# Kernel tuning notes

Measured on AMD Instinct MI355X. Metric: run time of the kernel, lower is better.

Reference implementation:

```python
import jax, jax.numpy as jnp
import numpy as np

LN_EPS = 1e-12


def setup_inputs() -> dict:
    key = jax.random.key(0)
    ks = jax.random.split(key, 6)
    B, S, H = 32, 512, 768
    P, K = 76, 64
    V, E = 50257, 768
    return {
        "sequence_data": jax.random.normal(ks[0], (B, S, H), dtype=jnp.float32),
        "masked_positions": jax.random.randint(ks[1], (B, P), 0, S, dtype=jnp.int64),
        "candidate_sets": jax.random.randint(ks[2], (B, P, K), 0, V, dtype=jnp.int64),
        "embedding_table": jax.random.normal(ks[3], (V, E), dtype=jnp.float32) * 0.02,
        "dense_w": jax.random.normal(ks[4], (H, E), dtype=jnp.float32) * (1.0 / np.sqrt(H)),
        "dense_b": jnp.zeros((E,), dtype=jnp.float32),
        "ln_gamma": jnp.ones((E,), dtype=jnp.float32),
        "ln_beta": jnp.zeros((E,), dtype=jnp.float32),
    }


def reference(sequence_data, masked_positions, candidate_sets, embedding_table,
              dense_w, dense_b, ln_gamma, ln_beta):
    # Gather masked positions: [B, P, H]
    gathered = jnp.take_along_axis(
        sequence_data, masked_positions[:, :, None], axis=1)
    # Dense (no activation), then LayerNorm (eps=1e-12)
    lm = jnp.einsum('bph,he->bpe', gathered, dense_w) + dense_b
    mu = jnp.mean(lm, axis=-1, keepdims=True)
    var = jnp.mean(jnp.square(lm - mu), axis=-1, keepdims=True)
    lm = (lm - mu) * jax.lax.rsqrt(var + LN_EPS) * ln_gamma + ln_beta
    # Candidate embedding gather: [B, P, K, E]
    cand = embedding_table[candidate_sets]
    # Inner products -> logits [B, P, K]
    logits = jnp.einsum('bpe,bpke->bpk', lm, cand)
    return logits
```

## Files before the change

### kernel.cpp

```cpp
#include <hip/hip_runtime.h>

typedef __attribute__((ext_vector_type(8))) short bf16x8;
typedef __attribute__((ext_vector_type(4))) float f32x4;

#define HH 768
#define EE 768
#define BB 32
#define SS 512
#define PP 76
#define KCAND 64
#define MM (BB * PP)

__device__ inline unsigned short f2bf(float f) {
    unsigned int u = __float_as_uint(f);
    u += 0x7fffu + ((u >> 16) & 1u);
    return (unsigned short)(u >> 16);
}

__global__ __launch_bounds__(256) void prep_kernel(
    const float* __restrict__ W, unsigned short* __restrict__ Wt,
    const float* __restrict__ seq, const int* __restrict__ mpos,
    unsigned short* __restrict__ Ag) {
    const int bid = blockIdx.x;
    if (bid < 576) {
        __shared__ float tile[32][33];
        const int h0 = (bid % 24) * 32, e0 = (bid / 24) * 32;
        const int c = threadIdx.x & 31, r = threadIdx.x >> 5;
#pragma unroll
        for (int rr = r; rr < 32; rr += 8)
            tile[rr][c] = W[(size_t)(h0 + rr) * EE + e0 + c];
        __syncthreads();
#pragma unroll
        for (int rr = r; rr < 32; rr += 8)
            Wt[(size_t)(e0 + rr) * HH + h0 + c] = f2bf(tile[c][rr]);
    } else {
        const int m0 = (bid - 576) * 8;
        const int t = threadIdx.x;
#pragma unroll
        for (int rr = 0; rr < 8; ++rr) {
            const int m = m0 + rr;
            const int b = m / PP, p = m - b * PP;
            const int ps = mpos[b * PP + p];
            const float* srow = seq + (size_t)(b * SS + ps) * HH;
            unsigned short* drow = Ag + (size_t)m * HH;
#pragma unroll
            for (int j = 0; j < 3; ++j) {
                const int idx = t + j * 256;
                drow[idx] = f2bf(srow[idx]);
            }
        }
    }
}

__global__ __launch_bounds__(256) void gemm_kernel(
    const unsigned short* __restrict__ Ag, const unsigned short* __restrict__ Wt,
    float* __restrict__ lm) {
    __shared__ unsigned short Alds[64][136];
    __shared__ unsigned short Blds[64][136];
    const int bm = blockIdx.y, bn = blockIdx.x;
    const int tid = threadIdx.x;
    const int sr = tid >> 4;
    const int sc = (tid & 15) * 8;
    const unsigned short* abase = Ag + (size_t)(bm * 64) * HH;
    const unsigned short* bbase = Wt + (size_t)(bn * 64) * HH;

    const int lane = tid & 63, wv = tid >> 6;
    const int wm = wv >> 1, wn = wv & 1;
    const int fr = lane & 15, fq = (lane >> 4) * 8;
    f32x4 acc[2][2] = {};

    for (int kk = 0; kk < HH; kk += 128) {
        __syncthreads();
#pragma unroll
        for (int rnd = 0; rnd < 4; ++rnd) {
            const int row = sr + rnd * 16;
            *(int4*)&Alds[row][sc] = *(const int4*)(abase + (size_t)row * HH + kk + sc);
            *(int4*)&Blds[row][sc] = *(const int4*)(bbase + (size_t)row * HH + kk + sc);
        }
        __syncthreads();
#pragma unroll
        for (int ks = 0; ks < 128; ks += 32) {
            bf16x8 af[2], bfr[2];
#pragma unroll
            for (int t = 0; t < 2; ++t)
                af[t] = *(const bf16x8*)&Alds[wm * 32 + t * 16 + fr][ks + fq];
#pragma unroll
            for (int t = 0; t < 2; ++t)
                bfr[t] = *(const bf16x8*)&Blds[wn * 32 + t * 16 + fr][ks + fq];
#pragma unroll
            for (int tm = 0; tm < 2; ++tm)
#pragma unroll
                for (int tn = 0; tn < 2; ++tn)
                    acc[tm][tn] = __builtin_amdgcn_mfma_f32_16x16x32_bf16(
                        af[tm], bfr[tn], acc[tm][tn], 0, 0, 0);
        }
    }
#pragma unroll
    for (int tm = 0; tm < 2; ++tm)
#pragma unroll
        for (int tn = 0; tn < 2; ++tn) {
            const int col = bn * 64 + wn * 32 + tn * 16 + (lane & 15);
            const int rbase = bm * 64 + wm * 32 + tm * 16 + (lane >> 4) * 4;
#pragma unroll
            for (int g = 0; g < 4; ++g)
                lm[(size_t)(rbase + g) * EE + col] = acc[tm][tn][g];
        }
}

__global__ __launch_bounds__(256) void logits_kernel(
    const float* __restrict__ lm, const float* __restrict__ bias,
    const float* __restrict__ gamma, const float* __restrict__ beta,
    const int* __restrict__ cand, const float* __restrict__ emb,
    float* __restrict__ out) {
    __shared__ float4 rowv4[192];
    __shared__ float reds[4], redq[4], stat[2];
    float* row = (float*)rowv4;
    const int bp = blockIdx.x;
    const int tid = threadIdx.x, lane = tid & 63, wv = tid >> 6;

    float s = 0.f, qq = 0.f;
    float v[3];
#pragma unroll
    for (int i = 0; i < 3; ++i) {
        const int idx = tid + i * 256;
        const float x = lm[(size_t)bp * EE + idx] + bias[idx];
        v[i] = x; s += x; qq += x * x;
    }
#pragma unroll
    for (int m = 32; m; m >>= 1) { s += __shfl_xor(s, m); qq += __shfl_xor(qq, m); }
    if (lane == 0) { reds[wv] = s; redq[wv] = qq; }
    __syncthreads();
    if (tid == 0) {
        const float S = reds[0] + reds[1] + reds[2] + reds[3];
        const float Q = redq[0] + redq[1] + redq[2] + redq[3];
        const float mu = S * (1.0f / 768.0f);
        const float var = Q * (1.0f / 768.0f) - mu * mu;
        stat[0] = mu; stat[1] = rsqrtf(var + 1e-12f);
    }
    __syncthreads();
    const float mu = stat[0], rstd = stat[1];
#pragma unroll
    for (int i = 0; i < 3; ++i) {
        const int idx = tid + i * 256;
        row[idx] = (v[i] - mu) * rstd * gamma[idx] + beta[idx];
    }
    __syncthreads();

    const float4 l0 = rowv4[lane], l1 = rowv4[lane + 64], l2 = rowv4[lane + 128];
#pragma unroll
    for (int it = 0; it < 4; ++it) {
        const int k0 = wv * 16 + it * 4;
        const float4* er[4];
#pragma unroll
        for (int c = 0; c < 4; ++c) {
            const int cid = cand[bp * KCAND + k0 + c];
            er[c] = (const float4*)(emb + (size_t)cid * EE);
        }
        float4 ra[4], rb[4], rc[4];
#pragma unroll
        for (int c = 0; c < 4; ++c) {
            ra[c] = er[c][lane]; rb[c] = er[c][lane + 64]; rc[c] = er[c][lane + 128];
        }
        float t[4];
#pragma unroll
        for (int c = 0; c < 4; ++c)
            t[c] = ra[c].x * l0.x + ra[c].y * l0.y + ra[c].z * l0.z + ra[c].w * l0.w
                 + rb[c].x * l1.x + rb[c].y * l1.y + rb[c].z * l1.z + rb[c].w * l1.w
                 + rc[c].x * l2.x + rc[c].y * l2.y + rc[c].z * l2.z + rc[c].w * l2.w;
#pragma unroll
        for (int m = 32; m; m >>= 1) {
#pragma unroll
            for (int c = 0; c < 4; ++c) t[c] += __shfl_xor(t[c], m);
        }
        if (lane == 0) {
#pragma unroll
            for (int c = 0; c < 4; ++c) out[bp * KCAND + k0 + c] = t[c];
        }
    }
}

extern "C" void kernel_launch(void* const* d_in, const int* in_sizes, int n_in,
                              void* d_out, int out_size, void* d_ws, size_t ws_size,
                              hipStream_t stream) {
    const float* seq   = (const float*)d_in[0];
    const int*   mpos  = (const int*)d_in[1];
    const int*   cand  = (const int*)d_in[2];
    const float* emb   = (const float*)d_in[3];
    const float* W     = (const float*)d_in[4];
    const float* bias  = (const float*)d_in[5];
    const float* gamma = (const float*)d_in[6];
    const float* beta  = (const float*)d_in[7];
    float* out = (float*)d_out;

    unsigned short* Wt = (unsigned short*)d_ws;
    unsigned short* Ag = (unsigned short*)((char*)d_ws + 1179648);
    float* lm = (float*)((char*)d_ws + 1179648 + 3735552);

    prep_kernel<<<880, 256, 0, stream>>>(W, Wt, seq, mpos, Ag);
    gemm_kernel<<<dim3(12, 38), 256, 0, stream>>>(Ag, Wt, lm);
    logits_kernel<<<MM, 256, 0, stream>>>(lm, bias, gamma, beta, cand, emb, out);
}
```

Before: 292.2 us.

## Convert embedding table to bf16 per call and gather bf16 rows in logits

Adds a prep stage that converts the full embedding table to bf16 in workspace, then the logits kernel gathers bf16 candidate rows with 16-byte loads, processing two candidates per wave pass with a remapped lane layout. This halves the bytes of the random candidate-row gathers. It adds a full-table conversion pass each call (reading and writing the entire table) and reduces dot-product input precision.

```diff
diff --git a/kernel.cpp b/kernel.cpp
--- a/kernel.cpp
+++ b/kernel.cpp
@@ -10,21 +10,45 @@
 #define PP 76
 #define KCAND 64
 #define MM (BB * PP)
+#define VV 50257
+
+#define CONV_BLOCKS 18847
+#define WT_BLOCKS 576
+#define GATH_BLOCKS 304
 
 __device__ inline unsigned short f2bf(float f) {
     unsigned int u = __float_as_uint(f);
     u += 0x7fffu + ((u >> 16) & 1u);
     return (unsigned short)(u >> 16);
 }
+__device__ inline float bf2f(short h) {
+    return __uint_as_float(((unsigned int)(unsigned short)h) << 16);
+}
+__device__ inline float dot8(bf16x8 c, const float4 m0, const float4 m1) {
+    return bf2f(c[0]) * m0.x + bf2f(c[1]) * m0.y + bf2f(c[2]) * m0.z + bf2f(c[3]) * m0.w
+         + bf2f(c[4]) * m1.x + bf2f(c[5]) * m1.y + bf2f(c[6]) * m1.z + bf2f(c[7]) * m1.w;
+}
 
 __global__ __launch_bounds__(256) void prep_kernel(
     const float* __restrict__ W, unsigned short* __restrict__ Wt,
     const float* __restrict__ seq, const int* __restrict__ mpos,
-    unsigned short* __restrict__ Ag) {
+    unsigned short* __restrict__ Ag,
+    const float* __restrict__ emb, unsigned short* __restrict__ embb) {
     const int bid = blockIdx.x;
-    if (bid < 576) {
+    if (bid < CONV_BLOCKS) {
+        const size_t i8 = ((size_t)bid * 256 + threadIdx.x) * 8;
+        if (i8 < (size_t)VV * EE) {
+            const float4 a = *(const float4*)(emb + i8);
+            const float4 b = *(const float4*)(emb + i8 + 4);
+            unsigned short t[8];
+            t[0] = f2bf(a.x); t[1] = f2bf(a.y); t[2] = f2bf(a.z); t[3] = f2bf(a.w);
+            t[4] = f2bf(b.x); t[5] = f2bf(b.y); t[6] = f2bf(b.z); t[7] = f2bf(b.w);
+            *(int4*)(embb + i8) = *(const int4*)t;
+        }
+    } else if (bid < CONV_BLOCKS + WT_BLOCKS) {
         __shared__ float tile[32][33];
-        const int h0 = (bid % 24) * 32, e0 = (bid / 24) * 32;
+        const int wb = bid - CONV_BLOCKS;
+        const int h0 = (wb % 24) * 32, e0 = (wb / 24) * 32;
         const int c = threadIdx.x & 31, r = threadIdx.x >> 5;
 #pragma unroll
         for (int rr = r; rr < 32; rr += 8)
@@ -34,7 +58,7 @@
         for (int rr = r; rr < 32; rr += 8)
             Wt[(size_t)(e0 + rr) * HH + h0 + c] = f2bf(tile[c][rr]);
     } else {
-        const int m0 = (bid - 576) * 8;
+        const int m0 = (bid - CONV_BLOCKS - WT_BLOCKS) * 8;
         const int t = threadIdx.x;
 #pragma unroll
         for (int rr = 0; rr < 8; ++rr) {
@@ -110,7 +134,7 @@
 __global__ __launch_bounds__(256) void logits_kernel(
     const float* __restrict__ lm, const float* __restrict__ bias,
     const float* __restrict__ gamma, const float* __restrict__ beta,
-    const int* __restrict__ cand, const float* __restrict__ emb,
+    const int* __restrict__ cand, const unsigned short* __restrict__ embb,
     float* __restrict__ out) {
     __shared__ float4 rowv4[192];
     __shared__ float reds[4], redq[4], stat[2];
@@ -146,35 +170,50 @@
     }
     __syncthreads();
 
-    const float4 l0 = rowv4[lane], l1 = rowv4[lane + 64], l2 = rowv4[lane + 128];
-#pragma unroll
-    for (int it = 0; it < 4; ++it) {
-        const int k0 = wv * 16 + it * 4;
-        const float4* er[4];
-#pragma unroll
-        for (int c = 0; c < 4; ++c) {
-            const int cid = cand[bp * KCAND + k0 + c];
-            er[c] = (const float4*)(emb + (size_t)cid * EE);
-        }
-        float4 ra[4], rb[4], rc[4];
-#pragma unroll
-        for (int c = 0; c < 4; ++c) {
-            ra[c] = er[c][lane]; rb[c] = er[c][lane + 64]; rc[c] = er[c][lane + 128];
-        }
-        float t[4];
-#pragma unroll
-        for (int c = 0; c < 4; ++c)
-            t[c] = ra[c].x * l0.x + ra[c].y * l0.y + ra[c].z * l0.z + ra[c].w * l0.w
-                 + rb[c].x * l1.x + rb[c].y * l1.y + rb[c].z * l1.z + rb[c].w * l1.w
-                 + rc[c].x * l2.x + rc[c].y * l2.y + rc[c].z * l2.z + rc[c].w * l2.w;
-#pragma unroll
-        for (int m = 32; m; m >>= 1) {
-#pragma unroll
-            for (int c = 0; c < 4; ++c) t[c] += __shfl_xor(t[c], m);
-        }
-        if (lane == 0) {
-#pragma unroll
-            for (int c = 0; c < 4; ++c) out[bp * KCAND + k0 + c] = t[c];
+    const int j = lane & 31;
+    const bool halflo = (lane < 32);
+    const float4 A0 = rowv4[2 * j],        A1 = rowv4[2 * j + 1];
+    const float4 B0 = rowv4[2 * (j + 32)], B1 = rowv4[2 * (j + 32) + 1];
+    const float4 C0 = rowv4[2 * (j + 64)], C1 = rowv4[2 * (j + 64) + 1];
+    const float4 M00 = halflo ? A0 : B0, M01 = halflo ? A1 : B1;
+    const float4 M10 = halflo ? C0 : A0, M11 = halflo ? C1 : A1;
+    const float4 M20 = halflo ? B0 : C0, M21 = halflo ? B1 : C1;
+
+    const int kbase = wv * 16;
+#pragma unroll
+    for (int grp = 0; grp < 2; ++grp) {
+        bf16x8 c[4][3];
+#pragma unroll
+        for (int pr = 0; pr < 4; ++pr) {
+            const int kp = kbase + grp * 8 + pr * 2;
+            const int ca = cand[bp * KCAND + kp];
+            const int cb = cand[bp * KCAND + kp + 1];
+            const unsigned short* rA = embb + (size_t)ca * EE;
+            const unsigned short* rB = embb + (size_t)cb * EE;
+            c[pr][0] = *(const bf16x8*)(rA + lane * 8);
+            const unsigned short* p1 = halflo ? (rA + (lane + 64) * 8)
+                                              : (rB + (lane - 32) * 8);
+            c[pr][1] = *(const bf16x8*)p1;
+            c[pr][2] = *(const bf16x8*)(rB + (lane + 32) * 8);
+        }
+#pragma unroll
+        for (int pr = 0; pr < 4; ++pr) {
+            const float d0 = dot8(c[pr][0], M00, M01);
+            const float d1 = dot8(c[pr][1], M10, M11);
+            const float d2 = dot8(c[pr][2], M20, M21);
+            const float t = halflo ? d1 : 0.f;
+            float sA = d0 + t;
+            float sB = d2 + (d1 - t);
+#pragma unroll
+            for (int m = 32; m; m >>= 1) {
+                sA += __shfl_xor(sA, m);
+                sB += __shfl_xor(sB, m);
+            }
+            if (lane == 0) {
+                const int kp = kbase + grp * 8 + pr * 2;
+                out[bp * KCAND + kp] = sA;
+                out[bp * KCAND + kp + 1] = sB;
+            }
         }
     }
 }
@@ -194,9 +233,11 @@
 
     unsigned short* Wt = (unsigned short*)d_ws;
     unsigned short* Ag = (unsigned short*)((char*)d_ws + 1179648);
-    float* lm = (float*)((char*)d_ws + 1179648 + 3735552);
-
-    prep_kernel<<<880, 256, 0, stream>>>(W, Wt, seq, mpos, Ag);
+    float* lm          = (float*)((char*)d_ws + 4915200);
+    unsigned short* embb = (unsigned short*)((char*)d_ws + 12386304);
+
+    prep_kernel<<<CONV_BLOCKS + WT_BLOCKS + GATH_BLOCKS, 256, 0, stream>>>(
+        W, Wt, seq, mpos, Ag, emb, embb);
     gemm_kernel<<<dim3(12, 38), 256, 0, stream>>>(Ag, Wt, lm);
-    logits_kernel<<<MM, 256, 0, stream>>>(lm, bias, gamma, beta, cand, emb, out);
-}
+    logits_kernel<<<MM, 256, 0, stream>>>(lm, bias, gamma, beta, cand, embb, out);
+}
```

Measured after the change: 302.7 us. 3.6% more time.

## Group candidate logits by embedding row via counting sort to read each row once

Applied to the files above, without the earlier changes.

Builds a histogram, a prefix scan and a scatter permutation of candidate ids. Each embedding row is then loaded once and dotted against every normalized hidden row that references it, instead of gathering the same rows repeatedly per (b,p). LayerNorm is split into its own kernel that writes bf16 rows, so the dot products now read bf16 activations. This adds several extra launches, a single-block scan and global atomics, and lowers the precision of the normalized activations.

```diff
diff --git a/kernel.cpp b/kernel.cpp
--- a/kernel.cpp
+++ b/kernel.cpp
@@ -10,19 +10,43 @@
 #define PP 76
 #define KCAND 64
 #define MM (BB * PP)
+#define VV 50257
+#define NC (MM * KCAND)
+
+#define OFF_WT     0u
+#define OFF_AG     1183744u
+#define OFF_LMRAW  4923392u
+#define OFF_LMN    12394496u
+#define OFF_COUNT  16130048u
+#define OFF_CURSOR (OFF_COUNT + 201028u)
+#define OFF_BASE   (OFF_CURSOR + 201028u)
+#define OFF_PERM   (OFF_BASE + 201028u)
+
+#define WT_BLOCKS 576
+#define AG_BLOCKS 304
+#define HIST_BLOCKS 152
 
 __device__ inline unsigned short f2bf(float f) {
     unsigned int u = __float_as_uint(f);
     u += 0x7fffu + ((u >> 16) & 1u);
     return (unsigned short)(u >> 16);
 }
+__device__ inline float bf2f(unsigned short h) {
+    return __uint_as_float(((unsigned int)h) << 16);
+}
+
+__global__ __launch_bounds__(256) void zero_kernel(int* p) {
+    const int i = blockIdx.x * 256 + threadIdx.x;
+    if (i < 2 * VV) p[i] = 0;
+}
 
 __global__ __launch_bounds__(256) void prep_kernel(
     const float* __restrict__ W, unsigned short* __restrict__ Wt,
     const float* __restrict__ seq, const int* __restrict__ mpos,
-    unsigned short* __restrict__ Ag) {
+    unsigned short* __restrict__ Ag,
+    const int* __restrict__ cand, int* __restrict__ count) {
     const int bid = blockIdx.x;
-    if (bid < 576) {
+    if (bid < WT_BLOCKS) {
         __shared__ float tile[32][33];
         const int h0 = (bid % 24) * 32, e0 = (bid / 24) * 32;
         const int c = threadIdx.x & 31, r = threadIdx.x >> 5;
@@ -33,8 +57,8 @@
 #pragma unroll
         for (int rr = r; rr < 32; rr += 8)
             Wt[(size_t)(e0 + rr) * HH + h0 + c] = f2bf(tile[c][rr]);
-    } else {
-        const int m0 = (bid - 576) * 8;
+    } else if (bid < WT_BLOCKS + AG_BLOCKS) {
+        const int m0 = (bid - WT_BLOCKS) * 8;
         const int t = threadIdx.x;
 #pragma unroll
         for (int rr = 0; rr < 8; ++rr) {
@@ -44,12 +68,46 @@
             const float* srow = seq + (size_t)(b * SS + ps) * HH;
             unsigned short* drow = Ag + (size_t)m * HH;
 #pragma unroll
-            for (int j = 0; j < 3; ++j) {
-                const int idx = t + j * 256;
-                drow[idx] = f2bf(srow[idx]);
-            }
-        }
-    }
+            for (int j = 0; j < 3; ++j)
+                drow[t + j * 256] = f2bf(srow[t + j * 256]);
+        }
+    } else {
+        const int h = bid - WT_BLOCKS - AG_BLOCKS;
+        const int i0 = (h * 256 + threadIdx.x) * 4;
+#pragma unroll
+        for (int j = 0; j < 4; ++j)
+            atomicAdd(&count[cand[i0 + j]], 1);
+    }
+}
+
+__global__ __launch_bounds__(1024) void scan_kernel(
+    const int* __restrict__ count, int* __restrict__ base, int* __restrict__ cursor) {
+    __shared__ int part[1024];
+    const int t = threadIdx.x;
+    const int lo = t * 50, hi = (lo + 50 < VV) ? lo + 50 : VV;
+    int s = 0;
+    for (int i = lo; i < hi; ++i) s += count[i];
+    part[t] = s;
+    __syncthreads();
+    for (int off = 1; off < 1024; off <<= 1) {
+        const int v = (t >= off) ? part[t - off] : 0;
+        __syncthreads();
+        part[t] += v;
+        __syncthreads();
+    }
+    int run = part[t] - s;
+    for (int i = lo; i < hi; ++i) {
+        base[i] = run; cursor[i] = run;
+        run += count[i];
+    }
+}
+
+__global__ __launch_bounds__(256) void scatter_kernel(
+    const int* __restrict__ cand, int* __restrict__ cursor, int* __restrict__ perm) {
+    const int i = blockIdx.x * 256 + threadIdx.x;
+    const int row = cand[i];
+    const int slot = atomicAdd(&cursor[row], 1);
+    perm[slot] = i;
 }
 
 __global__ __launch_bounds__(256) void gemm_kernel(
@@ -107,74 +165,99 @@
         }
 }
 
-__global__ __launch_bounds__(256) void logits_kernel(
+__global__ __launch_bounds__(256) void ln_kernel(
     const float* __restrict__ lm, const float* __restrict__ bias,
     const float* __restrict__ gamma, const float* __restrict__ beta,
-    const int* __restrict__ cand, const float* __restrict__ emb,
-    float* __restrict__ out) {
-    __shared__ float4 rowv4[192];
-    __shared__ float reds[4], redq[4], stat[2];
-    float* row = (float*)rowv4;
-    const int bp = blockIdx.x;
-    const int tid = threadIdx.x, lane = tid & 63, wv = tid >> 6;
-
-    float s = 0.f, qq = 0.f;
-    float v[3];
-#pragma unroll
-    for (int i = 0; i < 3; ++i) {
-        const int idx = tid + i * 256;
-        const float x = lm[(size_t)bp * EE + idx] + bias[idx];
-        v[i] = x; s += x; qq += x * x;
-    }
-#pragma unroll
-    for (int m = 32; m; m >>= 1) { s += __shfl_xor(s, m); qq += __shfl_xor(qq, m); }
-    if (lane == 0) { reds[wv] = s; redq[wv] = qq; }
-    __syncthreads();
-    if (tid == 0) {
-        const float S = reds[0] + reds[1] + reds[2] + reds[3];
-        const float Q = redq[0] + redq[1] + redq[2] + redq[3];
-        const float mu = S * (1.0f / 768.0f);
-        const float var = Q * (1.0f / 768.0f) - mu * mu;
-        stat[0] = mu; stat[1] = rsqrtf(var + 1e-12f);
-    }
-    __syncthreads();
-    const float mu = stat[0], rstd = stat[1];
-#pragma unroll
-    for (int i = 0; i < 3; ++i) {
-        const int idx = tid + i * 256;
-        row[idx] = (v[i] - mu) * rstd * gamma[idx] + beta[idx];
-    }
-    __syncthreads();
-
-    const float4 l0 = rowv4[lane], l1 = rowv4[lane + 64], l2 = rowv4[lane + 128];
-#pragma unroll
-    for (int it = 0; it < 4; ++it) {
-        const int k0 = wv * 16 + it * 4;
-        const float4* er[4];
-#pragma unroll
-        for (int c = 0; c < 4; ++c) {
-            const int cid = cand[bp * KCAND + k0 + c];
-            er[c] = (const float4*)(emb + (size_t)cid * EE);
-        }
-        float4 ra[4], rb[4], rc[4];
-#pragma unroll
-        for (int c = 0; c < 4; ++c) {
-            ra[c] = er[c][lane]; rb[c] = er[c][lane + 64]; rc[c] = er[c][lane + 128];
-        }
-        float t[4];
-#pragma unroll
-        for (int c = 0; c < 4; ++c)
-            t[c] = ra[c].x * l0.x + ra[c].y * l0.y + ra[c].z * l0.z + ra[c].w * l0.w
-                 + rb[c].x * l1.x + rb[c].y * l1.y + rb[c].z * l1.z + rb[c].w * l1.w
-                 + rc[c].x * l2.x + rc[c].y * l2.y + rc[c].z * l2.z + rc[c].w * l2.w;
-#pragma unroll
-        for (int m = 32; m; m >>= 1) {
-#pragma unroll
-            for (int c = 0; c < 4; ++c) t[c] += __shfl_xor(t[c], m);
+    unsigned short* __restrict__ lmn) {
+    const int lane = threadIdx.x & 63;
+    const int m = blockIdx.x * 4 + (threadIdx.x >> 6);
+    const float4* x4 = (const float4*)(lm + (size_t)m * EE);
+    const float4* b4 = (const float4*)bias;
+    const float4* g4 = (const float4*)gamma;
+    const float4* e4 = (const float4*)beta;
+    float x[12], g[12], e[12];
+    {
+        const float4 X0 = x4[lane * 2], X1 = x4[lane * 2 + 1], X2 = x4[128 + lane];
+        const float4 B0 = b4[lane * 2], B1 = b4[lane * 2 + 1], B2 = b4[128 + lane];
+        const float4 G0 = g4[lane * 2], G1 = g4[lane * 2 + 1], G2 = g4[128 + lane];
+        const float4 E0 = e4[lane * 2], E1 = e4[lane * 2 + 1], E2 = e4[128 + lane];
+        x[0]=X0.x+B0.x; x[1]=X0.y+B0.y; x[2]=X0.z+B0.z; x[3]=X0.w+B0.w;
+        x[4]=X1.x+B1.x; x[5]=X1.y+B1.y; x[6]=X1.z+B1.z; x[7]=X1.w+B1.w;
+        x[8]=X2.x+B2.x; x[9]=X2.y+B2.y; x[10]=X2.z+B2.z; x[11]=X2.w+B2.w;
+        g[0]=G0.x; g[1]=G0.y; g[2]=G0.z; g[3]=G0.w;
+        g[4]=G1.x; g[5]=G1.y; g[6]=G1.z; g[7]=G1.w;
+        g[8]=G2.x; g[9]=G2.y; g[10]=G2.z; g[11]=G2.w;
+        e[0]=E0.x; e[1]=E0.y; e[2]=E0.z; e[3]=E0.w;
+        e[4]=E1.x; e[5]=E1.y; e[6]=E1.z; e[7]=E1.w;
+        e[8]=E2.x; e[9]=E2.y; e[10]=E2.z; e[11]=E2.w;
+    }
+    float s = 0.f, q = 0.f;
+#pragma unroll
+    for (int i = 0; i < 12; ++i) { s += x[i]; q += x[i] * x[i]; }
+#pragma unroll
+    for (int m2 = 32; m2; m2 >>= 1) { s += __shfl_xor(s, m2); q += __shfl_xor(q, m2); }
+    const float mu = s * (1.0f / 768.0f);
+    const float rstd = rsqrtf(q * (1.0f / 768.0f) - mu * mu + 1e-12f);
+    unsigned short o8[8];
+#pragma unroll
+    for (int i = 0; i < 8; ++i) o8[i] = f2bf((x[i] - mu) * rstd * g[i] + e[i]);
+    *(int4*)(lmn + (size_t)m * EE + lane * 8) = *(const int4*)o8;
+    unsigned short o4[4];
+#pragma unroll
+    for (int i = 0; i < 4; ++i) o4[i] = f2bf((x[8 + i] - mu) * rstd * g[8 + i] + e[8 + i]);
+    *(ushort2*)(lmn + (size_t)m * EE + 512 + lane * 4) = *(const ushort2*)o4;
+    *(ushort2*)(lmn + (size_t)m * EE + 512 + lane * 4 + 2) = *(const ushort2*)(o4 + 2);
+}
+
+__global__ __launch_bounds__(256) void group_logits_kernel(
+    const float* __restrict__ emb, const unsigned short* __restrict__ lmn,
+    const int* __restrict__ count, const int* __restrict__ basep,
+    const int* __restrict__ perm, float* __restrict__ out) {
+    const int lane = threadIdx.x & 63;
+    const int r = blockIdx.x * 4 + (threadIdx.x >> 6);
+    if (r >= VV) return;
+    const int c = count[r];
+    if (c == 0) return;
+    const int base = basep[r];
+    const float4* e4 = (const float4*)(emb + (size_t)r * EE);
+    const float4 E0 = e4[lane * 2], E1 = e4[lane * 2 + 1], E2 = e4[128 + lane];
+    const int l8 = lane * 8, l4 = 512 + lane * 4;
+
+    for (int o = 0; o < c; o += 4) {
+        const int nn = c - o;
+        int idxv[4]; bf16x8 c8[4]; ushort4 c4v[4];
+#pragma unroll
+        for (int j = 0; j < 4; ++j) {
+            const int jj = (j < nn) ? j : 0;
+            const int idx = perm[base + o + jj];
+            idxv[j] = idx;
+            const unsigned short* lrow = lmn + (size_t)(idx >> 6) * EE;
+            c8[j] = *(const bf16x8*)(lrow + l8);
+            c4v[j] = *(const ushort4*)(lrow + l4);
+        }
+        float d[4];
+#pragma unroll
+        for (int j = 0; j < 4; ++j) {
+            d[j] = bf2f((unsigned short)c8[j][0]) * E0.x
+                 + bf2f((unsigned short)c8[j][1]) * E0.y
+                 + bf2f((unsigned short)c8[j][2]) * E0.z
+                 + bf2f((unsigned short)c8[j][3]) * E0.w
+                 + bf2f((unsigned short)c8[j][4]) * E1.x
+                 + bf2f((unsigned short)c8[j][5]) * E1.y
+                 + bf2f((unsigned short)c8[j][6]) * E1.z
+                 + bf2f((unsigned short)c8[j][7]) * E1.w
+                 + bf2f(c4v[j].x) * E2.x + bf2f(c4v[j].y) * E2.y
+                 + bf2f(c4v[j].z) * E2.z + bf2f(c4v[j].w) * E2.w;
+        }
+#pragma unroll
+        for (int m2 = 32; m2; m2 >>= 1) {
+#pragma unroll
+            for (int j = 0; j < 4; ++j) d[j] += __shfl_xor(d[j], m2);
         }
         if (lane == 0) {
 #pragma unroll
-            for (int c = 0; c < 4; ++c) out[bp * KCAND + k0 + c] = t[c];
+            for (int j = 0; j < 4; ++j)
+                if (j < nn) out[idxv[j]] = d[j];
         }
     }
 }
@@ -192,11 +275,22 @@
     const float* beta  = (const float*)d_in[7];
     float* out = (float*)d_out;
 
-    unsigned short* Wt = (unsigned short*)d_ws;
-    unsigned short* Ag = (unsigned short*)((char*)d_ws + 1179648);
-    float* lm = (float*)((char*)d_ws + 1179648 + 3735552);
-
-    prep_kernel<<<880, 256, 0, stream>>>(W, Wt, seq, mpos, Ag);
+    char* ws = (char*)d_ws;
+    unsigned short* Wt   = (unsigned short*)(ws + OFF_WT);
+    unsigned short* Ag   = (unsigned short*)(ws + OFF_AG);
+    float*          lm   = (float*)(ws + OFF_LMRAW);
+    unsigned short* lmn  = (unsigned short*)(ws + OFF_LMN);
+    int*            cnt  = (int*)(ws + OFF_COUNT);
+    int*            cur  = (int*)(ws + OFF_CURSOR);
+    int*            bse  = (int*)(ws + OFF_BASE);
+    int*            perm = (int*)(ws + OFF_PERM);
+
+    zero_kernel<<<(2 * VV + 255) / 256, 256, 0, stream>>>(cnt);
+    prep_kernel<<<WT_BLOCKS + AG_BLOCKS + HIST_BLOCKS, 256, 0, stream>>>(
+        W, Wt, seq, mpos, Ag, cand, cnt);
+    scan_kernel<<<1, 1024, 0, stream>>>(cnt, bse, cur);
+    scatter_kernel<<<NC / 256, 256, 0, stream>>>(cand, cur, perm);
     gemm_kernel<<<dim3(12, 38), 256, 0, stream>>>(Ag, Wt, lm);
-    logits_kernel<<<MM, 256, 0, stream>>>(lm, bias, gamma, beta, cand, emb, out);
-}
+    ln_kernel<<<MM / 4, 256, 0, stream>>>(lm, bias, gamma, beta, lmn);
+    group_logits_kernel<<<(VV + 3) / 4, 256, 0, stream>>>(emb, lmn, cnt, bse, perm, out);
+}
```

Result: slower. 394.8 us (+35.1%).
